# Kernel optimization log

Measured on AMD Instinct MI355X. Metric: run time of the kernel, lower is better.

## Reference

```python
import jax, jax.numpy as jnp
import numpy as np

BN_EPS = 1e-3


def _knn_group(p1, p2, k):
    # p1, p2: [B, N, 3]. For each point in p1, find k nearest in p2.
    d2 = (jnp.sum(p1 * p1, -1)[:, :, None]
          + jnp.sum(p2 * p2, -1)[:, None, :]
          - 2.0 * jnp.einsum('bnd,bmd->bnm', p1, p2))  # [B,N,N]
    _, idx = jax.lax.top_k(-d2, k)                      # [B,N,k]
    nn = jax.vmap(lambda pts, ind: pts[ind])(p2, idx)   # [B,N,k,3]
    resi = nn - p1[:, :, None, :]                       # [B,N,k,3]
    ss = jnp.sum(resi * resi, -1, keepdims=True)
    dist = jnp.sqrt(jnp.maximum(ss, 1e-12))             # safe norm
    feat = jnp.concatenate([resi, dist], -1)            # [B,N,k,4]
    return feat.transpose(0, 3, 1, 2), nn.transpose(0, 3, 1, 2)  # [B,4,N,k],[B,3,N,k]


def _conv_bn_relu(x, W, b, g, be, m, v):
    # 1x1 conv over channel dim: x [B,C,N,K], W [O,C]
    x = jnp.einsum('bcnk,oc->bonk', x, W) + b[None, :, None, None]
    x = (x - m[None, :, None, None]) * (g / jnp.sqrt(v + BN_EPS))[None, :, None, None] + be[None, :, None, None]
    return jax.nn.relu(x)


def setup_inputs() -> dict:
    key = jax.random.key(0)
    ks = jax.random.split(key, 20)
    B, N = 8, 2048
    chans = [4, 64, 64, 128]
    inp = {
        'points1': jax.random.normal(ks[0], (B, 3, N), jnp.float32),
        'points2': jax.random.normal(ks[1], (B, 3, N), jnp.float32),
    }
    for i in range(3):
        ci, co = chans[i], chans[i + 1]
        base = 2 + i * 6
        scale = 1.0 / np.sqrt(ci)
        inp[f'W{i+1}'] = jax.random.uniform(ks[base], (co, ci), jnp.float32, -scale, scale)
        inp[f'b{i+1}'] = jax.random.uniform(ks[base + 1], (co,), jnp.float32, -scale, scale)
        inp[f'g{i+1}'] = 1.0 + 0.1 * jax.random.normal(ks[base + 2], (co,), jnp.float32)
        inp[f'be{i+1}'] = 0.1 * jax.random.normal(ks[base + 3], (co,), jnp.float32)
        inp[f'm{i+1}'] = 0.05 * jax.random.normal(ks[base + 4], (co,), jnp.float32)
        inp[f'v{i+1}'] = jax.random.uniform(ks[base + 5], (co,), jnp.float32, 0.5, 1.5)
    inp['k'] = 32
    inp['t'] = 1
    return inp


def reference(points1, points2, W1, b1, g1, be1, m1, v1, W2, b2, g2, be2, m2, v2,
              W3, b3, g3, be3, m3, v3, k, t):
    p1 = points1.transpose(0, 2, 1)  # [B,N,3]
    p2 = points2.transpose(0, 2, 1)
    f1, nn1 = _knn_group(p1, p1, k)
    f2, nn2 = _knn_group(p1, p2, k)
    feats = jnp.concatenate([f1, f2], -1)          # [B,4,N,2k]
    grouped = jnp.concatenate([nn1, nn2], -1)      # [B,3,N,2k]
    x = _conv_bn_relu(feats, W1, b1, g1, be1, m1, v1)
    x = _conv_bn_relu(x, W2, b2, g2, be2, m2, v2)
    x = _conv_bn_relu(x, W3, b3, g3, be3, m3, v3)
    x = jnp.max(x, axis=1)                         # [B,N,2k] max over channels
    w = jax.nn.softmax(x, axis=-1)                 # softmax over 2k neighbors
    fused = jnp.sum(w[:, None, :, :] * grouped, -1)  # [B,3,N]
    return fused
```

## Files before the change

### kernel.cpp

```cpp
#include <hip/hip_runtime.h>
#include <hip/hip_bf16.h>
#include <stdint.h>

#define BB 8
#define NN 2048

#define OFF_B1 272
#define OFF_B2 4432
#define OFF_B3 12688
#define IDX_BYTE_OFF 65536
#define T_BASE   (65536 + 2*1024*1024)
#define T1_OFF   T_BASE
#define T2H_OFF  (T1_OFF + 4096)
#define T2L_OFF  (T2H_OFF + 9216)
#define T3H_OFF  (T2L_OFF + 9216)
#define T3L_OFF  (T3H_OFF + 18432)
#define L_T1   0
#define L_T2H  2048
#define L_T2L  6656
#define L_T3H  11264
#define L_T3L  20480
#define L_HALVES 29696

typedef __attribute__((ext_vector_type(4))) float f32x4;
typedef __attribute__((ext_vector_type(8))) short s16x8;

__device__ __forceinline__ float ldany(const void* p, long i, int isf32) {
    if (isf32) return ((const float*)p)[i];
    uint32_t u = ((uint32_t)((const uint16_t*)p)[i]) << 16;
    float f; __builtin_memcpy(&f, &u, 4); return f;
}
__device__ __forceinline__ uint16_t f2bf(float f) {
    uint32_t u; __builtin_memcpy(&u, &f, 4);
    return (uint16_t)((u + 0x7FFFu + ((u >> 16) & 1u)) >> 16);
}
__device__ __forceinline__ float bf2f(uint16_t h) {
    uint32_t u = ((uint32_t)h) << 16;
    float f; __builtin_memcpy(&f, &u, 4); return f;
}
__device__ __forceinline__ uint32_t pk2(float a, float b) {
    __hip_bfloat162 h = __float22bfloat162_rn(make_float2(a, b));
    uint32_t u; __builtin_memcpy(&u, &h, 4); return u;
}
__device__ __forceinline__ s16x8 mk8(uint32_t a, uint32_t b, uint32_t c, uint32_t d) {
    uint32_t t[4] = {a, b, c, d}; s16x8 r; __builtin_memcpy(&r, t, 16); return r;
}
__device__ __forceinline__ float sane(float v) {
    return (v == v && v > -1e30f && v < 1e30f) ? v : 0.f;
}
__device__ __forceinline__ int mbcnt64(unsigned long long m) {
    return __builtin_amdgcn_mbcnt_hi((uint32_t)(m >> 32),
           __builtin_amdgcn_mbcnt_lo((uint32_t)m, 0));
}
__device__ __forceinline__ int kperm_pos(int kk) {
    int g = kk >> 5, c5 = kk & 31;
    int sub = (c5 >> 4) & 1, q = (c5 >> 2) & 3, r = c5 & 3;
    return 32 * g + 8 * q + 4 * sub + r;
}

__global__ void k0_fold(const void* p1,
                        const void* W1, const void* b1, const void* g1, const void* be1, const void* m1, const void* v1,
                        const void* W2, const void* b2, const void* g2, const void* be2, const void* m2, const void* v2,
                        const void* W3, const void* b3, const void* g3, const void* be3, const void* m3, const void* v3,
                        float* wsf, int* wsi) {
    __shared__ int s_cnt;
    int t = threadIdx.x;
    if (t == 0) s_cnt = 0;
    __syncthreads();
    const uint16_t* u = (const uint16_t*)p1;
    int c = 0;
    for (int i = t; i < 4096; i += 256) {
        uint16_t x = u[i];
        uint32_t e = (x >> 7) & 0xFF;
        c += ((e >= 0x70 && e <= 0x84) || x == 0) ? 1 : 0;
    }
    atomicAdd(&s_cnt, c);
    __syncthreads();
    int isf32 = (s_cnt < 3686) ? 1 : 0;
    if (blockIdx.x == 0 && t == 0) wsi[0] = isf32;

    uint16_t* t1  = (uint16_t*)((char*)wsf + T1_OFF);
    uint16_t* t2h = (uint16_t*)((char*)wsf + T2H_OFF);
    uint16_t* t2l = (uint16_t*)((char*)wsf + T2L_OFF);
    uint16_t* t3h = (uint16_t*)((char*)wsf + T3H_OFF);
    uint16_t* t3l = (uint16_t*)((char*)wsf + T3L_OFF);

    int gid = blockIdx.x * 256 + t;
    if (gid < 4096) {
        int o = gid >> 6, kk = gid & 63;
        float s = ldany(g2, o, isf32) * rsqrtf(ldany(v2, o, isf32) + 1e-3f);
        float w = ldany(W2, gid, isf32) * s;
        uint16_t wh = f2bf(w);
        int pos = o * 72 + kperm_pos(kk);
        t2h[pos] = wh; t2l[pos] = f2bf(w - bf2f(wh));
    } else if (gid < 12288) {
        int e = gid - 4096;
        int o = e >> 6, kk = e & 63;
        float s = ldany(g3, o, isf32) * rsqrtf(ldany(v3, o, isf32) + 1e-3f);
        float w = ldany(W3, e, isf32) * s;
        uint16_t wh = f2bf(w);
        int pos = o * 72 + kperm_pos(kk);
        t3h[pos] = wh; t3l[pos] = f2bf(w - bf2f(wh));
    } else if (gid < 12544) {
        int e = gid - 12288;
        int co = e >> 2, cc = e & 3;
        float s = ldany(g1, co, isf32) * rsqrtf(ldany(v1, co, isf32) + 1e-3f);
        float w = ldany(W1, co*4 + cc, isf32) * s;
        uint16_t wh = f2bf(w), wl = f2bf(w - bf2f(wh));
        t1[co*32 + cc]     = wh;
        t1[co*32 + 4 + cc] = wh;
        t1[co*32 + 8 + cc] = wl;
    } else if (gid < 13824) {
        int e = gid - 12544;
        int co = e / 20, k = e - co * 20;
        t1[co*32 + 12 + k] = 0;
    } else if (gid < 13888) {
        int o = gid - 13824;
        float s = ldany(g1, o, isf32) * rsqrtf(ldany(v1, o, isf32) + 1e-3f);
        wsf[OFF_B1 + o] = (ldany(b1, o, isf32) - ldany(m1, o, isf32)) * s + ldany(be1, o, isf32);
    } else if (gid < 13952) {
        int o = gid - 13888;
        float s = ldany(g2, o, isf32) * rsqrtf(ldany(v2, o, isf32) + 1e-3f);
        wsf[OFF_B2 + o] = (ldany(b2, o, isf32) - ldany(m2, o, isf32)) * s + ldany(be2, o, isf32);
    } else if (gid < 14080) {
        int o = gid - 13952;
        float s = ldany(g3, o, isf32) * rsqrtf(ldany(v3, o, isf32) + 1e-3f);
        wsf[OFF_B3 + o] = (ldany(b3, o, isf32) - ldany(m3, o, isf32)) * s + ldany(be3, o, isf32);
    }
}

__device__ __forceinline__ void knn_target(const void* p, long base, int isf32, int lane,
                                           float qx, float qy, float qz, float s1,
                                           unsigned long long* sl, uint16_t* dst) {
    uint32_t kb[32];
    if (!isf32) {
        const uint16_t* tpu = (const uint16_t*)p + base;
        const uint4* rx = (const uint4*)(tpu);
        const uint4* ry = (const uint4*)(tpu + NN);
        const uint4* rz = (const uint4*)(tpu + 2*NN);
        #pragma unroll
        for (int i = 0; i < 4; i++) {
            int v4 = i * 64 + lane;
            uint4 X = rx[v4], Y = ry[v4], Z = rz[v4];
            uint32_t xw[4] = {X.x, X.y, X.z, X.w};
            uint32_t yw[4] = {Y.x, Y.y, Y.z, Y.w};
            uint32_t zw[4] = {Z.x, Z.y, Z.z, Z.w};
            #pragma unroll
            for (int j = 0; j < 4; j++) {
                #pragma unroll
                for (int w = 0; w < 2; w++) {
                    uint32_t ux = (w == 0) ? (xw[j] << 16) : (xw[j] & 0xFFFF0000u);
                    uint32_t uy = (w == 0) ? (yw[j] << 16) : (yw[j] & 0xFFFF0000u);
                    uint32_t uz = (w == 0) ? (zw[j] << 16) : (zw[j] & 0xFFFF0000u);
                    float nx, ny, nz;
                    __builtin_memcpy(&nx, &ux, 4); __builtin_memcpy(&ny, &uy, 4); __builtin_memcpy(&nz, &uz, 4);
                    float s2  = nx * nx + ny * ny + nz * nz;
                    float dot = qx * nx + qy * ny + qz * nz;
                    float d2  = fmaxf((s1 + s2) - 2.0f * dot, 0.0f);
                    uint32_t bits; __builtin_memcpy(&bits, &d2, 4);
                    kb[i*8 + j*2 + w] = bits;
                }
            }
        }
    } else {
        const float* tpf = (const float*)p + base;
        #pragma unroll
        for (int i = 0; i < 32; i++) {
            int j = i * 64 + lane;
            float nx = tpf[j];
            float ny = tpf[NN + j];
            float nz = tpf[2*NN + j];
            float s2  = nx * nx + ny * ny + nz * nz;
            float dot = qx * nx + qy * ny + qz * nz;
            float d2  = fmaxf((s1 + s2) - 2.0f * dot, 0.0f);
            uint32_t bits; __builtin_memcpy(&bits, &d2, 4);
            kb[i] = bits;
        }
    }

    uint32_t lo = 0u, hi = 0x7F800001u, tau = 0u;
    uint32_t mid = 0x3E800000u;
    while (true) {
        int c = 0;
        #pragma unroll
        for (int i = 0; i < 32; i++) c += __builtin_popcountll(__ballot(kb[i] < mid));
        if (c < 32)      lo = mid;
        else if (c > 64) hi = mid;
        else { tau = mid; break; }
        if (hi - lo <= 1u) { tau = hi; break; }
        mid = lo + ((hi - lo) >> 1);
    }

    sl[lane] = ~0ull;
    int basePos = 0;
    #pragma unroll
    for (int i = 0; i < 32; i++) {
        unsigned idxv = isf32 ? (unsigned)(i * 64 + lane)
                              : (unsigned)((i >> 3) * 512 + 8 * lane + (i & 7));
        bool pz = kb[i] < tau;
        unsigned long long m = __ballot(pz);
        int pos = basePos + mbcnt64(m);
        if (pz && pos < 64) sl[pos] = (((unsigned long long)kb[i]) << 32) | idxv;
        basePos += __builtin_popcountll(m);
    }
    unsigned long long key = sl[lane];

    #pragma unroll
    for (int sz = 2; sz <= 64; sz <<= 1) {
        #pragma unroll
        for (int st = sz >> 1; st > 0; st >>= 1) {
            unsigned long long ot = __shfl_xor(key, st, 64);
            bool up    = ((lane & sz) == 0);
            bool lower = ((lane & st) == 0);
            unsigned long long mn = (key < ot) ? key : ot;
            unsigned long long mx = (key < ot) ? ot : key;
            key = (lower == up) ? mn : mx;
        }
    }

    if (lane < 32) dst[lane] = (uint16_t)(key & 0x7FFu);
}

__launch_bounds__(256)
__global__ void k1_knn(const void* p1, const void* p2, const int* wsi, uint16_t* idxout) {
    __shared__ unsigned long long smem[4 * 64];

    int isf32 = wsi[0];
    int lane = threadIdx.x & 63;
    int wave = threadIdx.x >> 6;
    int qidx = blockIdx.x * 4 + wave;
    int b = qidx >> 11, n = qidx & 2047;
    long base = (long)b * 3 * NN;

    float qx = ldany(p1, base + n,        isf32);
    float qy = ldany(p1, base + NN + n,   isf32);
    float qz = ldany(p1, base + 2*NN + n, isf32);
    float s1 = qx * qx + qy * qy + qz * qz;

    unsigned long long* sl = smem + wave * 64;
    long obase = ((long)qidx) << 6;

    knn_target(p1, base, isf32, lane, qx, qy, qz, s1, sl, idxout + obase);

    __builtin_amdgcn_sched_barrier(0);
    asm volatile("" ::: "memory");

    knn_target(p2, base, isf32, lane, qx, qy, qz, s1, sl, idxout + obase + 32);
}

__launch_bounds__(512)
__global__ void k2_mlp(const void* p1, const void* p2, const float* __restrict__ wsf, const int* wsi,
                       const uint16_t* __restrict__ idxin, void* outp) {
    __shared__ uint4 shw4[L_HALVES / 8];

    {
        const uint4* src = (const uint4*)((const char*)wsf + T1_OFF);
        for (int i = threadIdx.x; i < L_HALVES / 8; i += 512) shw4[i] = src[i];
    }
    __syncthreads();
    const uint16_t* shw = (const uint16_t*)shw4;
    const uint16_t* T1  = shw + L_T1;
    const uint16_t* T2H = shw + L_T2H;
    const uint16_t* T2L = shw + L_T2L;
    const uint16_t* T3H = shw + L_T3H;
    const uint16_t* T3L = shw + L_T3L;

    int isf32 = wsi[0];
    int lane = threadIdx.x & 63;
    int wave = threadIdx.x >> 6;
    int c = lane & 15;
    int q = lane >> 4;
    int qidx = blockIdx.x * 8 + wave;
    int b = qidx >> 11, n = qidx & 2047;
    long base = (long)b * 3 * NN;

    float qx = sane(ldany(p1, base + n,        isf32));
    float qy = sane(ldany(p1, base + NN + n,   isf32));
    float qz = sane(ldany(p1, base + 2*NN + n, isf32));

    int idx = idxin[((long)qidx << 6) + lane] & 2047;
    const void* sp = (lane < 32) ? p1 : p2;
    float nx = sane(ldany(sp, base + idx,        isf32));
    float ny = sane(ldany(sp, base + NN + idx,   isf32));
    float nz = sane(ldany(sp, base + 2*NN + idx, isf32));

    float r0 = nx - qx, r1 = ny - qy, r2 = nz - qz;
    float ss = fmaf(r0, r0, fmaf(r1, r1, r2 * r2));
    float dist = sqrtf(fmaxf(ss, 1e-12f));

    const float* B1 = wsf + OFF_B1;
    const float* B2 = wsf + OFF_B2;
    const float* B3 = wsf + OFF_B3;

    s16x8 b1f[4];
    #pragma unroll
    for (int nt = 0; nt < 4; nt++) {
        int src = 16 * nt + c;
        float f0 = __shfl(r0, src, 64);
        float f1 = __shfl(r1, src, 64);
        float f2v = __shfl(r2, src, 64);
        float f3v = __shfl(dist, src, 64);
        uint16_t h0 = f2bf(f0), h1 = f2bf(f1), h2 = f2bf(f2v), h3 = f2bf(f3v);
        uint16_t l0 = f2bf(f0 - bf2f(h0)), l1 = f2bf(f1 - bf2f(h1));
        uint16_t l2 = f2bf(f2v - bf2f(h2)), l3 = f2bf(f3v - bf2f(h3));
        s16x8 v;
        bool qa = (q < 2);
        bool qb = (q == 0);
        v[0] = qa ? (short)h0 : (short)0;
        v[1] = qa ? (short)h1 : (short)0;
        v[2] = qa ? (short)h2 : (short)0;
        v[3] = qa ? (short)h3 : (short)0;
        v[4] = qb ? (short)l0 : (short)0;
        v[5] = qb ? (short)l1 : (short)0;
        v[6] = qb ? (short)l2 : (short)0;
        v[7] = qb ? (short)l3 : (short)0;
        b1f[nt] = v;
    }

    f32x4 d1[4][4];
    #pragma unroll
    for (int mt = 0; mt < 4; mt++) {
        s16x8 a1 = *(const s16x8*)(T1 + (16 * mt + c) * 32 + q * 8);
        f32x4 bias = *(const f32x4*)(B1 + 16 * mt + 4 * q);
        #pragma unroll
        for (int nt = 0; nt < 4; nt++) {
            d1[mt][nt] = __builtin_amdgcn_mfma_f32_16x16x32_bf16(a1, b1f[nt], bias, 0, 0, 0);
        }
    }

    auto mkfrag = [](const f32x4& dlo, const f32x4& dhi) -> s16x8 {
        return mk8(pk2(fmaxf(dlo[0], 0.f), fmaxf(dlo[1], 0.f)),
                   pk2(fmaxf(dlo[2], 0.f), fmaxf(dlo[3], 0.f)),
                   pk2(fmaxf(dhi[0], 0.f), fmaxf(dhi[1], 0.f)),
                   pk2(fmaxf(dhi[2], 0.f), fmaxf(dhi[3], 0.f)));
    };

    f32x4 d2[4][4];
    #pragma unroll
    for (int mt = 0; mt < 4; mt++) {
        f32x4 bias = *(const f32x4*)(B2 + 16 * mt + 4 * q);
        #pragma unroll
        for (int nt = 0; nt < 4; nt++) d2[mt][nt] = bias;
    }
    #pragma unroll
    for (int g = 0; g < 2; g++) {
        s16x8 fh[4];
        #pragma unroll
        for (int nt = 0; nt < 4; nt++) fh[nt] = mkfrag(d1[2*g][nt], d1[2*g+1][nt]);
        #pragma unroll
        for (int mt = 0; mt < 4; mt++) {
            s16x8 ah = *(const s16x8*)(T2H + (16 * mt + c) * 72 + 32 * g + 8 * q);
            s16x8 al = *(const s16x8*)(T2L + (16 * mt + c) * 72 + 32 * g + 8 * q);
            #pragma unroll
            for (int nt = 0; nt < 4; nt++) {
                f32x4 acc = d2[mt][nt];
                acc = __builtin_amdgcn_mfma_f32_16x16x32_bf16(ah, fh[nt], acc, 0, 0, 0);
                acc = __builtin_amdgcn_mfma_f32_16x16x32_bf16(al, fh[nt], acc, 0, 0, 0);
                d2[mt][nt] = acc;
            }
        }
    }

    s16x8 f3h[2][4];
    #pragma unroll
    for (int g = 0; g < 2; g++)
        #pragma unroll
        for (int nt = 0; nt < 4; nt++) f3h[g][nt] = mkfrag(d2[2*g][nt], d2[2*g+1][nt]);

    float mx[4] = {-1e30f, -1e30f, -1e30f, -1e30f};
    #pragma unroll
    for (int mt = 0; mt < 8; mt++) {
        f32x4 bias = *(const f32x4*)(B3 + 16 * mt + 4 * q);
        f32x4 acc[4];
        #pragma unroll
        for (int nt = 0; nt < 4; nt++) acc[nt] = bias;
        #pragma unroll
        for (int g = 0; g < 2; g++) {
            s16x8 ah = *(const s16x8*)(T3H + (16 * mt + c) * 72 + 32 * g + 8 * q);
            s16x8 al = *(const s16x8*)(T3L + (16 * mt + c) * 72 + 32 * g + 8 * q);
            #pragma unroll
            for (int nt = 0; nt < 4; nt++) {
                f32x4 a = acc[nt];
                a = __builtin_amdgcn_mfma_f32_16x16x32_bf16(ah, f3h[g][nt], a, 0, 0, 0);
                a = __builtin_amdgcn_mfma_f32_16x16x32_bf16(al, f3h[g][nt], a, 0, 0, 0);
                acc[nt] = a;
            }
        }
        #pragma unroll
        for (int nt = 0; nt < 4; nt++) {
            mx[nt] = fmaxf(mx[nt], fmaxf(fmaxf(acc[nt][0], acc[nt][1]), fmaxf(acc[nt][2], acc[nt][3])));
        }
    }

    #pragma unroll
    for (int nt = 0; nt < 4; nt++) {
        mx[nt] = fmaxf(mx[nt], __shfl_xor(mx[nt], 16, 64));
        mx[nt] = fmaxf(mx[nt], __shfl_xor(mx[nt], 32, 64));
        mx[nt] = fmaxf(mx[nt], 0.f);
    }
    float mall = fmaxf(fmaxf(mx[0], mx[1]), fmaxf(mx[2], mx[3]));
    #pragma unroll
    for (int m = 1; m < 16; m <<= 1) mall = fmaxf(mall, __shfl_xor(mall, m, 64));
    float e0 = __expf(mx[0] - mall), e1 = __expf(mx[1] - mall);
    float e2 = __expf(mx[2] - mall), e3 = __expf(mx[3] - mall);
    float s = e0 + e1 + e2 + e3;
    #pragma unroll
    for (int m = 1; m < 16; m <<= 1) s += __shfl_xor(s, m, 64);
    float eown = (q == 0) ? e0 : (q == 1) ? e1 : (q == 2) ? e2 : e3;
    float w = eown / s;

    float sx = w * nx, sy = w * ny, sz = w * nz;
    #pragma unroll
    for (int m = 1; m < 64; m <<= 1) {
        sx += __shfl_xor(sx, m, 64);
        sy += __shfl_xor(sy, m, 64);
        sz += __shfl_xor(sz, m, 64);
    }

    if (lane < 3) {
        float v = (lane == 0) ? sx : ((lane == 1) ? sy : sz);
        long oi = base + (long)lane * NN + n;
        if (isf32) {
            ((float*)outp)[oi] = v;
        } else {
            ((uint16_t*)outp)[oi] = f2bf(v);
        }
    }
}

extern "C" void kernel_launch(void* const* d_in, const int* in_sizes, int n_in,
                              void* d_out, int out_size, void* d_ws, size_t ws_size,
                              hipStream_t stream) {
    const void* p1 = d_in[0];
    const void* p2 = d_in[1];
    float* wsf = (float*)d_ws;
    int*   wsi = (int*)d_ws;
    uint16_t* idxbuf = (uint16_t*)((char*)d_ws + IDX_BYTE_OFF);

    k0_fold<<<64, 256, 0, stream>>>(p1,
        d_in[2],  d_in[3],  d_in[4],  d_in[5],  d_in[6],  d_in[7],
        d_in[8],  d_in[9],  d_in[10], d_in[11], d_in[12], d_in[13],
        d_in[14], d_in[15], d_in[16], d_in[17], d_in[18], d_in[19],
        wsf, wsi);

    k1_knn<<<(BB * NN) / 4, 256, 0, stream>>>(p1, p2, wsi, idxbuf);

    k2_mlp<<<(BB * NN) / 8, 512, 0, stream>>>(p1, p2, wsf, wsi, idxbuf, d_out);
}
```

Before: 259.8 us.

## Interleave both KNN searches per wave and precompute target squared norms

The two sequential per-target KNN passes (self and cross) are merged into one interleaved pass. Distances for both targets are computed together, the bisection threshold searches run jointly, and the compaction and bitonic sorts are interleaved to expose more instruction-level parallelism. Squared norms of all target points are now computed once in the fold kernel and read from workspace in the bf16 path. The cost is doubled register arrays (64 keys per lane), with launch bounds set to 3 waves/SIMD, plus possible spills and lower occupancy. The joint bisection also keeps looping until both searches finish, adding extra branch overhead.

```diff
diff --git a/kernel.cpp b/kernel.cpp
--- a/kernel.cpp
+++ b/kernel.cpp
@@ -15,6 +15,7 @@
 #define T2L_OFF  (T2H_OFF + 9216)
 #define T3H_OFF  (T2L_OFF + 9216)
 #define T3L_OFF  (T3H_OFF + 18432)
+#define S2_OFF   2228224
 #define L_T1   0
 #define L_T2H  2048
 #define L_T2L  6656
@@ -58,7 +59,7 @@
     return 32 * g + 8 * q + 4 * sub + r;
 }
 
-__global__ void k0_fold(const void* p1,
+__global__ void k0_fold(const void* p1, const void* p2,
                         const void* W1, const void* b1, const void* g1, const void* be1, const void* m1, const void* v1,
                         const void* W2, const void* b2, const void* g2, const void* be2, const void* m2, const void* v2,
                         const void* W3, const void* b3, const void* g3, const void* be3, const void* m3, const void* v3,
@@ -84,8 +85,21 @@
     uint16_t* t2l = (uint16_t*)((char*)wsf + T2L_OFF);
     uint16_t* t3h = (uint16_t*)((char*)wsf + T3H_OFF);
     uint16_t* t3l = (uint16_t*)((char*)wsf + T3L_OFF);
+    float*    s2o = (float*)((char*)wsf + S2_OFF);
 
     int gid = blockIdx.x * 256 + t;
+
+    for (int e = gid; e < 32768; e += 16384) {
+        int tgt = e >> 14; int rem = e & 16383;
+        int b = rem >> 11, n = rem & 2047;
+        const void* pp = tgt ? p2 : p1;
+        long bb = (long)b * 3 * NN;
+        float x = ldany(pp, bb + n,        isf32);
+        float y = ldany(pp, bb + NN + n,   isf32);
+        float z = ldany(pp, bb + 2*NN + n, isf32);
+        s2o[e] = fmaf(x, x, fmaf(y, y, z * z));
+    }
+
     if (gid < 4096) {
         int o = gid >> 6, kk = gid & 63;
         float s = ldany(g2, o, isf32) * rsqrtf(ldany(v2, o, isf32) + 1e-3f);
@@ -129,101 +143,10 @@
     }
 }
 
-__device__ __forceinline__ void knn_target(const void* p, long base, int isf32, int lane,
-                                           float qx, float qy, float qz, float s1,
-                                           unsigned long long* sl, uint16_t* dst) {
-    uint32_t kb[32];
-    if (!isf32) {
-        const uint16_t* tpu = (const uint16_t*)p + base;
-        const uint4* rx = (const uint4*)(tpu);
-        const uint4* ry = (const uint4*)(tpu + NN);
-        const uint4* rz = (const uint4*)(tpu + 2*NN);
-        #pragma unroll
-        for (int i = 0; i < 4; i++) {
-            int v4 = i * 64 + lane;
-            uint4 X = rx[v4], Y = ry[v4], Z = rz[v4];
-            uint32_t xw[4] = {X.x, X.y, X.z, X.w};
-            uint32_t yw[4] = {Y.x, Y.y, Y.z, Y.w};
-            uint32_t zw[4] = {Z.x, Z.y, Z.z, Z.w};
-            #pragma unroll
-            for (int j = 0; j < 4; j++) {
-                #pragma unroll
-                for (int w = 0; w < 2; w++) {
-                    uint32_t ux = (w == 0) ? (xw[j] << 16) : (xw[j] & 0xFFFF0000u);
-                    uint32_t uy = (w == 0) ? (yw[j] << 16) : (yw[j] & 0xFFFF0000u);
-                    uint32_t uz = (w == 0) ? (zw[j] << 16) : (zw[j] & 0xFFFF0000u);
-                    float nx, ny, nz;
-                    __builtin_memcpy(&nx, &ux, 4); __builtin_memcpy(&ny, &uy, 4); __builtin_memcpy(&nz, &uz, 4);
-                    float s2  = nx * nx + ny * ny + nz * nz;
-                    float dot = qx * nx + qy * ny + qz * nz;
-                    float d2  = fmaxf((s1 + s2) - 2.0f * dot, 0.0f);
-                    uint32_t bits; __builtin_memcpy(&bits, &d2, 4);
-                    kb[i*8 + j*2 + w] = bits;
-                }
-            }
-        }
-    } else {
-        const float* tpf = (const float*)p + base;
-        #pragma unroll
-        for (int i = 0; i < 32; i++) {
-            int j = i * 64 + lane;
-            float nx = tpf[j];
-            float ny = tpf[NN + j];
-            float nz = tpf[2*NN + j];
-            float s2  = nx * nx + ny * ny + nz * nz;
-            float dot = qx * nx + qy * ny + qz * nz;
-            float d2  = fmaxf((s1 + s2) - 2.0f * dot, 0.0f);
-            uint32_t bits; __builtin_memcpy(&bits, &d2, 4);
-            kb[i] = bits;
-        }
-    }
-
-    uint32_t lo = 0u, hi = 0x7F800001u, tau = 0u;
-    uint32_t mid = 0x3E800000u;
-    while (true) {
-        int c = 0;
-        #pragma unroll
-        for (int i = 0; i < 32; i++) c += __builtin_popcountll(__ballot(kb[i] < mid));
-        if (c < 32)      lo = mid;
-        else if (c > 64) hi = mid;
-        else { tau = mid; break; }
-        if (hi - lo <= 1u) { tau = hi; break; }
-        mid = lo + ((hi - lo) >> 1);
-    }
-
-    sl[lane] = ~0ull;
-    int basePos = 0;
-    #pragma unroll
-    for (int i = 0; i < 32; i++) {
-        unsigned idxv = isf32 ? (unsigned)(i * 64 + lane)
-                              : (unsigned)((i >> 3) * 512 + 8 * lane + (i & 7));
-        bool pz = kb[i] < tau;
-        unsigned long long m = __ballot(pz);
-        int pos = basePos + mbcnt64(m);
-        if (pz && pos < 64) sl[pos] = (((unsigned long long)kb[i]) << 32) | idxv;
-        basePos += __builtin_popcountll(m);
-    }
-    unsigned long long key = sl[lane];
-
-    #pragma unroll
-    for (int sz = 2; sz <= 64; sz <<= 1) {
-        #pragma unroll
-        for (int st = sz >> 1; st > 0; st >>= 1) {
-            unsigned long long ot = __shfl_xor(key, st, 64);
-            bool up    = ((lane & sz) == 0);
-            bool lower = ((lane & st) == 0);
-            unsigned long long mn = (key < ot) ? key : ot;
-            unsigned long long mx = (key < ot) ? ot : key;
-            key = (lower == up) ? mn : mx;
-        }
-    }
-
-    if (lane < 32) dst[lane] = (uint16_t)(key & 0x7FFu);
-}
-
-__launch_bounds__(256)
-__global__ void k1_knn(const void* p1, const void* p2, const int* wsi, uint16_t* idxout) {
-    __shared__ unsigned long long smem[4 * 64];
+__launch_bounds__(256, 3)
+__global__ void k1_knn(const void* p1, const void* p2, const float* __restrict__ s2g,
+                       const int* wsi, uint16_t* idxout) {
+    __shared__ unsigned long long smem[4][2][64];
 
     int isf32 = wsi[0];
     int lane = threadIdx.x & 63;
@@ -237,15 +160,168 @@
     float qz = ldany(p1, base + 2*NN + n, isf32);
     float s1 = qx * qx + qy * qy + qz * qz;
 
-    unsigned long long* sl = smem + wave * 64;
+    uint32_t kb1[32], kb2[32];
+
+    if (!isf32) {
+        const uint16_t* u1 = (const uint16_t*)p1 + base;
+        const uint16_t* u2 = (const uint16_t*)p2 + base;
+        const uint4* rx1 = (const uint4*)(u1);
+        const uint4* ry1 = (const uint4*)(u1 + NN);
+        const uint4* rz1 = (const uint4*)(u1 + 2*NN);
+        const uint4* rx2 = (const uint4*)(u2);
+        const uint4* ry2 = (const uint4*)(u2 + NN);
+        const uint4* rz2 = (const uint4*)(u2 + 2*NN);
+        const f32x4* sA4 = (const f32x4*)(s2g + b * 2048);
+        const f32x4* sB4 = (const f32x4*)(s2g + 16384 + b * 2048);
+        #pragma unroll
+        for (int i = 0; i < 4; i++) {
+            int v4 = i * 64 + lane;
+            uint4 X1 = rx1[v4], Y1 = ry1[v4], Z1 = rz1[v4];
+            uint4 X2 = rx2[v4], Y2 = ry2[v4], Z2 = rz2[v4];
+            f32x4 SA0 = sA4[i*128 + 2*lane], SA1 = sA4[i*128 + 2*lane + 1];
+            f32x4 SB0 = sB4[i*128 + 2*lane], SB1 = sB4[i*128 + 2*lane + 1];
+            uint32_t x1w[4] = {X1.x, X1.y, X1.z, X1.w};
+            uint32_t y1w[4] = {Y1.x, Y1.y, Y1.z, Y1.w};
+            uint32_t z1w[4] = {Z1.x, Z1.y, Z1.z, Z1.w};
+            uint32_t x2w[4] = {X2.x, X2.y, X2.z, X2.w};
+            uint32_t y2w[4] = {Y2.x, Y2.y, Y2.z, Y2.w};
+            uint32_t z2w[4] = {Z2.x, Z2.y, Z2.z, Z2.w};
+            #pragma unroll
+            for (int j = 0; j < 4; j++) {
+                #pragma unroll
+                for (int w = 0; w < 2; w++) {
+                    int r = j * 2 + w;
+                    {
+                        uint32_t ux = (w == 0) ? (x1w[j] << 16) : (x1w[j] & 0xFFFF0000u);
+                        uint32_t uy = (w == 0) ? (y1w[j] << 16) : (y1w[j] & 0xFFFF0000u);
+                        uint32_t uz = (w == 0) ? (z1w[j] << 16) : (z1w[j] & 0xFFFF0000u);
+                        float nx, ny, nz;
+                        __builtin_memcpy(&nx, &ux, 4); __builtin_memcpy(&ny, &uy, 4); __builtin_memcpy(&nz, &uz, 4);
+                        float s2v = (r < 4) ? SA0[r] : SA1[r - 4];
+                        float dot = fmaf(qx, nx, fmaf(qy, ny, qz * nz));
+                        float d2  = fmaxf(fmaf(-2.0f, dot, s1 + s2v), 0.0f);
+                        uint32_t bits; __builtin_memcpy(&bits, &d2, 4);
+                        kb1[i*8 + r] = bits;
+                    }
+                    {
+                        uint32_t ux = (w == 0) ? (x2w[j] << 16) : (x2w[j] & 0xFFFF0000u);
+                        uint32_t uy = (w == 0) ? (y2w[j] << 16) : (y2w[j] & 0xFFFF0000u);
+                        uint32_t uz = (w == 0) ? (z2w[j] << 16) : (z2w[j] & 0xFFFF0000u);
+                        float nx, ny, nz;
+                        __builtin_memcpy(&nx, &ux, 4); __builtin_memcpy(&ny, &uy, 4); __builtin_memcpy(&nz, &uz, 4);
+                        float s2v = (r < 4) ? SB0[r] : SB1[r - 4];
+                        float dot = fmaf(qx, nx, fmaf(qy, ny, qz * nz));
+                        float d2  = fmaxf(fmaf(-2.0f, dot, s1 + s2v), 0.0f);
+                        uint32_t bits; __builtin_memcpy(&bits, &d2, 4);
+                        kb2[i*8 + r] = bits;
+                    }
+                }
+            }
+        }
+    } else {
+        const float* t1f = (const float*)p1 + base;
+        const float* t2f = (const float*)p2 + base;
+        #pragma unroll
+        for (int i = 0; i < 32; i++) {
+            int j = i * 64 + lane;
+            {
+                float nx = t1f[j], ny = t1f[NN + j], nz = t1f[2*NN + j];
+                float s2  = nx * nx + ny * ny + nz * nz;
+                float dot = qx * nx + qy * ny + qz * nz;
+                float d2  = fmaxf((s1 + s2) - 2.0f * dot, 0.0f);
+                uint32_t bits; __builtin_memcpy(&bits, &d2, 4);
+                kb1[i] = bits;
+            }
+            {
+                float nx = t2f[j], ny = t2f[NN + j], nz = t2f[2*NN + j];
+                float s2  = nx * nx + ny * ny + nz * nz;
+                float dot = qx * nx + qy * ny + qz * nz;
+                float d2  = fmaxf((s1 + s2) - 2.0f * dot, 0.0f);
+                uint32_t bits; __builtin_memcpy(&bits, &d2, 4);
+                kb2[i] = bits;
+            }
+        }
+    }
+
+    uint32_t lo1 = 0u, hi1 = 0x7F800001u, tau1 = 0u, mid1 = 0x3E800000u;
+    uint32_t lo2 = 0u, hi2 = 0x7F800001u, tau2 = 0u, mid2 = 0x3E800000u;
+    bool fin1 = false, fin2 = false;
+    while (!(fin1 && fin2)) {
+        int c1 = 0, c2 = 0;
+        if (!fin1) {
+            #pragma unroll
+            for (int i = 0; i < 32; i++) c1 += __builtin_popcountll(__ballot(kb1[i] < mid1));
+        }
+        if (!fin2) {
+            #pragma unroll
+            for (int i = 0; i < 32; i++) c2 += __builtin_popcountll(__ballot(kb2[i] < mid2));
+        }
+        if (!fin1) {
+            if (c1 < 32)      lo1 = mid1;
+            else if (c1 > 64) hi1 = mid1;
+            else { tau1 = mid1; fin1 = true; }
+            if (!fin1) {
+                if (hi1 - lo1 <= 1u) { tau1 = hi1; fin1 = true; }
+                else mid1 = lo1 + ((hi1 - lo1) >> 1);
+            }
+        }
+        if (!fin2) {
+            if (c2 < 32)      lo2 = mid2;
+            else if (c2 > 64) hi2 = mid2;
+            else { tau2 = mid2; fin2 = true; }
+            if (!fin2) {
+                if (hi2 - lo2 <= 1u) { tau2 = hi2; fin2 = true; }
+                else mid2 = lo2 + ((hi2 - lo2) >> 1);
+            }
+        }
+    }
+
+    unsigned long long* sl1 = &smem[wave][0][0];
+    unsigned long long* sl2 = &smem[wave][1][0];
+    sl1[lane] = ~0ull;
+    sl2[lane] = ~0ull;
+    int bp1 = 0, bp2 = 0;
+    #pragma unroll
+    for (int i = 0; i < 32; i++) {
+        unsigned idxv = isf32 ? (unsigned)(i * 64 + lane)
+                              : (unsigned)((i >> 3) * 512 + 8 * lane + (i & 7));
+        bool pz1 = kb1[i] < tau1;
+        unsigned long long m1 = __ballot(pz1);
+        int pos1 = bp1 + mbcnt64(m1);
+        if (pz1 && pos1 < 64) sl1[pos1] = (((unsigned long long)kb1[i]) << 32) | idxv;
+        bp1 += __builtin_popcountll(m1);
+
+        bool pz2 = kb2[i] < tau2;
+        unsigned long long m2 = __ballot(pz2);
+        int pos2 = bp2 + mbcnt64(m2);
+        if (pz2 && pos2 < 64) sl2[pos2] = (((unsigned long long)kb2[i]) << 32) | idxv;
+        bp2 += __builtin_popcountll(m2);
+    }
+    unsigned long long key1 = sl1[lane];
+    unsigned long long key2 = sl2[lane];
+
+    #pragma unroll
+    for (int sz = 2; sz <= 64; sz <<= 1) {
+        #pragma unroll
+        for (int st = sz >> 1; st > 0; st >>= 1) {
+            unsigned long long ot1 = __shfl_xor(key1, st, 64);
+            unsigned long long ot2 = __shfl_xor(key2, st, 64);
+            bool up    = ((lane & sz) == 0);
+            bool lower = ((lane & st) == 0);
+            unsigned long long mn1 = (key1 < ot1) ? key1 : ot1;
+            unsigned long long mx1 = (key1 < ot1) ? ot1 : key1;
+            key1 = (lower == up) ? mn1 : mx1;
+            unsigned long long mn2 = (key2 < ot2) ? key2 : ot2;
+            unsigned long long mx2 = (key2 < ot2) ? ot2 : key2;
+            key2 = (lower == up) ? mn2 : mx2;
+        }
+    }
+
     long obase = ((long)qidx) << 6;
-
-    knn_target(p1, base, isf32, lane, qx, qy, qz, s1, sl, idxout + obase);
-
-    __builtin_amdgcn_sched_barrier(0);
-    asm volatile("" ::: "memory");
-
-    knn_target(p2, base, isf32, lane, qx, qy, qz, s1, sl, idxout + obase + 32);
+    if (lane < 32) {
+        idxout[obase + lane]      = (uint16_t)(key1 & 0x7FFu);
+        idxout[obase + 32 + lane] = (uint16_t)(key2 & 0x7FFu);
+    }
 }
 
 __launch_bounds__(512)
@@ -436,14 +512,15 @@
     float* wsf = (float*)d_ws;
     int*   wsi = (int*)d_ws;
     uint16_t* idxbuf = (uint16_t*)((char*)d_ws + IDX_BYTE_OFF);
-
-    k0_fold<<<64, 256, 0, stream>>>(p1,
+    const float* s2g = (const float*)((char*)d_ws + S2_OFF);
+
+    k0_fold<<<64, 256, 0, stream>>>(p1, p2,
         d_in[2],  d_in[3],  d_in[4],  d_in[5],  d_in[6],  d_in[7],
         d_in[8],  d_in[9],  d_in[10], d_in[11], d_in[12], d_in[13],
         d_in[14], d_in[15], d_in[16], d_in[17], d_in[18], d_in[19],
         wsf, wsi);
 
-    k1_knn<<<(BB * NN) / 4, 256, 0, stream>>>(p1, p2, wsi, idxbuf);
+    k1_knn<<<(BB * NN) / 4, 256, 0, stream>>>(p1, p2, s2g, wsi, idxbuf);
 
     k2_mlp<<<(BB * NN) / 8, 512, 0, stream>>>(p1, p2, wsf, wsi, idxbuf, d_out);
 }
```

New measurement: 308.1 us. +18.6%, slower.
